# Kernel tuning notes

Hardware: AMD Instinct MI355X
Metric: run time of the kernel (lower is better)

The kernel has to match this reference:

```python
import jax, jax.numpy as jnp
import numpy as np

B, L, C, D = 8, 8192, 256, 256


def setup_inputs() -> dict:
    key = jax.random.key(0)
    ks = jax.random.split(key, 13)
    bound = 1.0 / np.sqrt(C)

    def W(k):
        return jax.random.uniform(k, (C, D), jnp.float32, -bound, bound)

    def b(k):
        return jax.random.uniform(k, (D,), jnp.float32, -bound, bound)

    return {
        "xs": jax.random.normal(ks[0], (B, L, C), jnp.float32),
        # forward-direction params
        "Wh1": W(ks[1]), "bh1": b(ks[2]),
        "Wz1": W(ks[3]), "bz1": b(ks[4]),
        "Ws1": W(ks[5]), "bs1": b(ks[6]),
        "h01": jnp.zeros((1, 1, D), jnp.float32),
        # backward-direction params
        "Wh_1": W(ks[7]), "bh_1": b(ks[8]),
        "Wz_1": W(ks[9]), "bz_1": b(ks[10]),
        "Ws_1": W(ks[11]), "bs_1": b(ks[12]),
        "h0_1": jnp.zeros((1, 1, D), jnp.float32),
    }


def _gru_scan(z, h_tilde, h0):
    """h[t] = z[t]*h_tilde[t] + (1-z[t])*h[t-1], h[-1]=h0. Parallel over time
    via associative scan on the affine maps h -> a*h + b."""
    a = 1.0 - z            # [B, L, D]
    b = z * h_tilde        # [B, L, D]

    def combine(c1, c2):
        a1, b1 = c1
        a2, b2 = c2
        return a1 * a2, a2 * b1 + b2

    A, Bc = jax.lax.associative_scan(combine, (a, b), axis=1)
    return Bc + A * h0     # broadcast h0 [1,1,D]


def reference(xs, Wh1, bh1, Wz1, bz1, Ws1, bs1, h01,
              Wh_1, bh_1, Wz_1, bz_1, Ws_1, bs_1, h0_1):
    sig = jax.nn.sigmoid
    # forward direction
    hf = _gru_scan(sig(xs @ Wz1 + bz1), xs @ Wh1 + bh1, h01) * sig(xs @ Ws1 + bs1)
    # backward direction: reverse time, scan, reverse back
    zr = sig(xs @ Wz_1 + bz_1)
    hr = xs @ Wh_1 + bh_1
    hb = _gru_scan(zr[:, ::-1], hr[:, ::-1], h0_1)[:, ::-1] * sig(xs @ Ws_1 + bs_1)
    return hf + hb
```

## Files before the change

### kernel.cpp

```cpp
#include <hip/hip_runtime.h>
#include <hip/hip_bf16.h>

typedef unsigned short u16;

#define BDIM 8
#define LDIM 8192
#define KDIM 256
#define DDIM 256
#define MTOT 65536
#define NDIM 1536
#define TCH  32
#define NCH  256


typedef float floatx4 __attribute__((ext_vector_type(4)));
typedef short bf16x8 __attribute__((ext_vector_type(8)));

__device__ __forceinline__ u16 f2bf(float f) {
  union { __hip_bfloat16 h; u16 u; } c;
  c.h = __float2bfloat16(f);
  return c.u;
}
__device__ __forceinline__ float bf2f(u16 u) {
  union { unsigned int i; float f; } c;
  c.i = ((unsigned int)u) << 16;
  return c.f;
}
__device__ __forceinline__ float sigmoidf_fast(float x) {
  return __builtin_amdgcn_rcpf(1.0f + __expf(-x));
}
__device__ __forceinline__ void gll16(const u16* g, u16* l) {
  __builtin_amdgcn_global_load_lds((const __attribute__((address_space(1))) void*)g,
                                   (__attribute__((address_space(3))) void*)l, 16, 0, 0);
}

__global__ void prep_weights(const float* __restrict__ Wh1, const float* __restrict__ Wz1,
                             const float* __restrict__ Ws1, const float* __restrict__ Wh_1,
                             const float* __restrict__ Wz_1, const float* __restrict__ Ws_1,
                             const float* __restrict__ bh1, const float* __restrict__ bz1,
                             const float* __restrict__ bs1, const float* __restrict__ bh_1,
                             const float* __restrict__ bz_1, const float* __restrict__ bs_1,
                             u16* __restrict__ WcatT, float* __restrict__ bcat) {
  const int n = blockIdx.x;
  const int k = threadIdx.x;
  const int dir = n / 768, r = n % 768;
  int d; const float* W; const float* bb;
  if (r < 512) {
    d = r >> 1;
    if (r & 1) { W = dir ? Wz_1 : Wz1; bb = dir ? bz_1 : bz1; }
    else       { W = dir ? Wh_1 : Wh1; bb = dir ? bh_1 : bh1; }
  } else {
    d = r - 512;
    W = dir ? Ws_1 : Ws1; bb = dir ? bs_1 : bs1;
  }
  WcatT[(size_t)n * KDIM + k] = f2bf(W[k * DDIM + d]);
  if (k == 0) bcat[n] = bb[d];
}

__global__ void convert_xs(const float* __restrict__ xs, u16* __restrict__ Abf) {
  size_t i = ((size_t)blockIdx.x * 256 + threadIdx.x) * 8;
  const float4* s = (const float4*)(xs + i);
  float4 f0 = s[0], f1 = s[1];
  union { u16 u[8]; uint4 v; } t;
  t.u[0] = f2bf(f0.x); t.u[1] = f2bf(f0.y); t.u[2] = f2bf(f0.z); t.u[3] = f2bf(f0.w);
  t.u[4] = f2bf(f1.x); t.u[5] = f2bf(f1.y); t.u[6] = f2bf(f1.z); t.u[7] = f2bf(f1.w);
  *(uint4*)(Abf + i) = t.v;
}

__global__ __launch_bounds__(256) void gemm_kernel(const u16* __restrict__ Abf,
                                                   const u16* __restrict__ WcatT,
                                                   const float* __restrict__ bcat,
                                                   u16* __restrict__ G) {
  __shared__ __align__(16) u16 As[8192];
  __shared__ __align__(16) u16 Bs[8192];
  const int tid = threadIdx.x;
  const int lane = tid & 63, wave = tid >> 6;
  const int wm = wave >> 1, wn = wave & 1;
  const int q = lane >> 4, r = lane & 15;

  const int xcd = blockIdx.x & 7;
  const int li  = blockIdx.x >> 3;
  const int mt  = xcd * 64 + li / 12;
  const int nt  = li % 12;
  const int m0 = mt * 128, n0 = nt * 128;

  const u16* gA[4]; const u16* gB[4]; u16* lA[4]; u16* lB[4];
#pragma unroll
  for (int j = 0; j < 4; j++) {
    const int bi = wave * 256 + j * 64 + lane;
    const int row = bi >> 3;
    const int kq = (bi & 7) ^ (row & 7);
    gA[j] = Abf   + (size_t)(m0 + row) * KDIM + kq * 8;
    gB[j] = WcatT + (size_t)(n0 + row) * KDIM + kq * 8;
    lA[j] = As + bi * 8;
    lB[j] = Bs + bi * 8;
  }

  floatx4 acc[4][4];
  floatx4 z4 = {0.f, 0.f, 0.f, 0.f};
#pragma unroll
  for (int i = 0; i < 4; i++)
#pragma unroll
    for (int j = 0; j < 4; j++) acc[i][j] = z4;

  for (int k0 = 0; k0 < KDIM; k0 += 64) {
#pragma unroll
    for (int j = 0; j < 4; j++) { gll16(gA[j] + k0, lA[j]); gll16(gB[j] + k0, lB[j]); }
    __syncthreads();
#pragma unroll
    for (int kk = 0; kk < 2; kk++) {
      bf16x8 af[4], bv[4];
#pragma unroll
      for (int i = 0; i < 4; i++) {
        const int row = wm * 64 + i * 16 + r;
        af[i] = *(const bf16x8*)(As + (row * 8 + ((kk * 4 + q) ^ (row & 7))) * 8);
      }
#pragma unroll
      for (int j = 0; j < 4; j++) {
        const int row = wn * 64 + j * 16 + r;
        bv[j] = *(const bf16x8*)(Bs + (row * 8 + ((kk * 4 + q) ^ (row & 7))) * 8);
      }
#pragma unroll
      for (int i = 0; i < 4; i++)
#pragma unroll
        for (int j = 0; j < 4; j++)
          acc[i][j] = __builtin_amdgcn_mfma_f32_16x16x32_bf16(af[i], bv[j], acc[i][j], 0, 0, 0);
    }
    __syncthreads();
  }

  float bvals[4];
#pragma unroll
  for (int j = 0; j < 4; j++) bvals[j] = bcat[n0 + wn * 64 + j * 16 + r];
#pragma unroll
  for (int i = 0; i < 4; i++) {
#pragma unroll
    for (int reg = 0; reg < 4; reg++) {
      size_t grow = (size_t)(m0 + wm * 64 + i * 16 + q * 4 + reg);
      u16* dst = G + grow * NDIM + n0 + wn * 64 + r;
#pragma unroll
      for (int j = 0; j < 4; j++)
        dst[j * 16] = f2bf(acc[i][j][reg] + bvals[j]);
    }
  }
}

__global__ __launch_bounds__(256) void scan_phaseA(const u16* __restrict__ G,
                                                   float* __restrict__ Acc,
                                                   float* __restrict__ Bcc) {
  const int slot = threadIdx.x >> 6, lane = threadIdx.x & 63;
  const int w = blockIdx.x * 4 + slot;
  const int u = w >> 1, half = w & 1;
  const int c = u & 255, b = (u >> 8) & 7, dir = u >> 11;
  const int d0 = half * 128 + lane * 2;
  const u16* p0 = G + (size_t)b * LDIM * NDIM + dir * 768 + d0 * 2;
  float h0 = 0.f, h1 = 0.f, P0 = 1.f, P1 = 1.f;
#pragma unroll 4
  for (int i = 0; i < TCH; ++i) {
    const int t = dir ? (c * TCH + (TCH - 1 - i)) : (c * TCH + i);
    uint2 hz = *(const uint2*)(p0 + (size_t)t * NDIM);
    const u16* q = (const u16*)&hz;
    float z0 = sigmoidf_fast(bf2f(q[1]));
    float z1 = sigmoidf_fast(bf2f(q[3]));
    float a0 = 1.f - z0, a1 = 1.f - z1;
    h0 = fmaf(a0, h0, z0 * bf2f(q[0]));
    h1 = fmaf(a1, h1, z1 * bf2f(q[2]));
    P0 *= a0; P1 *= a1;
  }
  float2 v;
  v.x = P0; v.y = P1;
  *(float2*)(Acc + (size_t)u * 256 + d0) = v;
  v.x = h0; v.y = h1;
  *(float2*)(Bcc + (size_t)u * 256 + d0) = v;
}

__global__ void scan_phaseB(const float* __restrict__ Acc, const float* __restrict__ Bcc,
                            const float* __restrict__ h01, const float* __restrict__ h0_1,
                            float* __restrict__ Pref) {
  const int d = threadIdx.x, b = blockIdx.x, dir = blockIdx.y;
  float h = dir ? h0_1[d] : h01[d];
  const size_t ubase = ((size_t)dir * BDIM + b) * NCH;
  if (dir == 0) {
    for (int c0 = 0; c0 < NCH; c0 += 8) {
      float a[8], bb[8];
#pragma unroll
      for (int j = 0; j < 8; ++j) {
        size_t idx = (ubase + c0 + j) * DDIM + d;
        a[j] = Acc[idx]; bb[j] = Bcc[idx];
      }
#pragma unroll
      for (int j = 0; j < 8; ++j) {
        Pref[(ubase + c0 + j) * DDIM + d] = h;
        h = fmaf(a[j], h, bb[j]);
      }
    }
  } else {
    for (int c0 = NCH - 1; c0 >= 0; c0 -= 8) {
      float a[8], bb[8];
#pragma unroll
      for (int j = 0; j < 8; ++j) {
        size_t idx = (ubase + c0 - j) * DDIM + d;
        a[j] = Acc[idx]; bb[j] = Bcc[idx];
      }
#pragma unroll
      for (int j = 0; j < 8; ++j) {
        Pref[(ubase + c0 - j) * DDIM + d] = h;
        h = fmaf(a[j], h, bb[j]);
      }
    }
  }
}

__global__ __launch_bounds__(512) void scan_phaseC(const u16* __restrict__ G,
                                                   const float* __restrict__ Pref,
                                                   float* __restrict__ out) {
  __shared__ float obuf[TCH * 256];
  const int c = blockIdx.x & 255, b = blockIdx.x >> 8;
  const int wave = threadIdx.x >> 6, lane = threadIdx.x & 63;
  const int dir = wave >> 2;
  const int d0 = (wave & 3) * 64 + lane;
  const int u = dir * 2048 + b * 256 + c;
  float h = Pref[(size_t)u * 256 + d0];
  const u16* ghz = G + (size_t)b * LDIM * NDIM + dir * 768 + d0 * 2;
  const u16* gs  = G + (size_t)b * LDIM * NDIM + dir * 768 + 512 + d0;

  if (dir == 1) {
#pragma unroll
    for (int i = 0; i < TCH; ++i) {
      const int tl = TCH - 1 - i;
      const int t = c * TCH + tl;
      unsigned int hz = *(const unsigned int*)(ghz + (size_t)t * NDIM);
      u16 sv = gs[(size_t)t * NDIM];
      float z = sigmoidf_fast(bf2f((u16)(hz >> 16)));
      h = fmaf(1.f - z, h, z * bf2f((u16)(hz & 0xffff)));
      obuf[tl * 256 + d0] = h * sigmoidf_fast(bf2f(sv));
    }
    __syncthreads();
  } else {
    float ov[TCH];
#pragma unroll
    for (int i = 0; i < TCH; ++i) {
      const int t = c * TCH + i;
      unsigned int hz = *(const unsigned int*)(ghz + (size_t)t * NDIM);
      u16 sv = gs[(size_t)t * NDIM];
      float z = sigmoidf_fast(bf2f((u16)(hz >> 16)));
      h = fmaf(1.f - z, h, z * bf2f((u16)(hz & 0xffff)));
      ov[i] = h * sigmoidf_fast(bf2f(sv));
    }
    __syncthreads();
#pragma unroll
    for (int i = 0; i < TCH; ++i) {
      const int t = c * TCH + i;
      out[((size_t)b * LDIM + t) * DDIM + d0] = ov[i] + obuf[i * 256 + d0];
    }
  }
}

extern "C" void kernel_launch(void* const* d_in, const int* in_sizes, int n_in,
                              void* d_out, int out_size, void* d_ws, size_t ws_size,
                              hipStream_t stream) {
  const float* xs   = (const float*)d_in[0];
  const float* Wh1  = (const float*)d_in[1];
  const float* bh1  = (const float*)d_in[2];
  const float* Wz1  = (const float*)d_in[3];
  const float* bz1  = (const float*)d_in[4];
  const float* Ws1  = (const float*)d_in[5];
  const float* bs1  = (const float*)d_in[6];
  const float* h01  = (const float*)d_in[7];
  const float* Wh_1 = (const float*)d_in[8];
  const float* bh_1 = (const float*)d_in[9];
  const float* Wz_1 = (const float*)d_in[10];
  const float* bz_1 = (const float*)d_in[11];
  const float* Ws_1 = (const float*)d_in[12];
  const float* bs_1 = (const float*)d_in[13];
  const float* h0_1 = (const float*)d_in[14];
  float* out = (float*)d_out;

  char* ws = (char*)d_ws;
  u16* WcatT = (u16*)ws;   ws += (size_t)NDIM * KDIM * 2;
  float* bcat = (float*)ws; ws += (size_t)NDIM * 4;
  u16* Abf = (u16*)ws;     ws += (size_t)MTOT * KDIM * 2;
  u16* G = (u16*)ws;       ws += (size_t)MTOT * NDIM * 2;
  float* Acc  = (float*)Abf;
  float* Bcc  = Acc + (size_t)2 * BDIM * NCH * DDIM;
  float* Pref = Bcc + (size_t)2 * BDIM * NCH * DDIM;
  if ((size_t)(ws - (char*)d_ws) > ws_size) return;

  prep_weights<<<dim3(NDIM), dim3(KDIM), 0, stream>>>(
      Wh1, Wz1, Ws1, Wh_1, Wz_1, Ws_1, bh1, bz1, bs1, bh_1, bz_1, bs_1, WcatT, bcat);
  convert_xs<<<dim3(MTOT * KDIM / (256 * 8)), dim3(256), 0, stream>>>(xs, Abf);
  gemm_kernel<<<dim3(6144), dim3(256), 0, stream>>>(Abf, WcatT, bcat, G);
  scan_phaseA<<<dim3(2048), dim3(256), 0, stream>>>(G, Acc, Bcc);
  scan_phaseB<<<dim3(BDIM, 2), dim3(DDIM), 0, stream>>>(Acc, Bcc, h01, h0_1, Pref);
  scan_phaseC<<<dim3(2048), dim3(512), 0, stream>>>(G, Pref, out);
}
```

Baseline: 298.8 us.

## Fuse chunk-local scan phase A into GEMM epilogue with permuted weight columns

Permutes the concatenated weight columns so each lane's four MFMA outputs are contiguous, which allows vectorized uint2 stores of G and a float4 bias load. For h/z column tiles, the GEMM epilogue also stages the bf16 tile in shared memory and computes the per-chunk scan products and offsets directly. This removes the separate scan_phaseA launch and its re-read of G. In exchange it adds a shared-memory pass and a serial 32-step loop to the epilogue of those tiles. It only runs when the workspace has room for separate Acc/Bcc buffers.

After: 284.2 us. 1.05x faster.

```diff
diff --git a/kernel.cpp b/kernel.cpp
--- a/kernel.cpp
+++ b/kernel.cpp
@@ -43,7 +43,9 @@
                              u16* __restrict__ WcatT, float* __restrict__ bcat) {
   const int n = blockIdx.x;
   const int k = threadIdx.x;
-  const int dir = n / 768, r = n % 768;
+  const int nn = n & 63;
+  const int p = (n & ~63) | ((nn & 15) << 2) | (nn >> 4);
+  const int dir = p / 768, r = p % 768;
   int d; const float* W; const float* bb;
   if (r < 512) {
     d = r >> 1;
@@ -54,7 +56,7 @@
     W = dir ? Ws_1 : Ws1; bb = dir ? bs_1 : bs1;
   }
   WcatT[(size_t)n * KDIM + k] = f2bf(W[k * DDIM + d]);
-  if (k == 0) bcat[n] = bb[d];
+  if (k == 0) bcat[p] = bb[d];
 }
 
 __global__ void convert_xs(const float* __restrict__ xs, u16* __restrict__ Abf) {
@@ -70,9 +72,13 @@
 __global__ __launch_bounds__(256) void gemm_kernel(const u16* __restrict__ Abf,
                                                    const u16* __restrict__ WcatT,
                                                    const float* __restrict__ bcat,
-                                                   u16* __restrict__ G) {
-  __shared__ __align__(16) u16 As[8192];
-  __shared__ __align__(16) u16 Bs[8192];
+                                                   u16* __restrict__ G,
+                                                   float* __restrict__ Acc,
+                                                   float* __restrict__ Bcc,
+                                                   int fuse) {
+  __shared__ __align__(16) u16 sm[16384];
+  u16* As = sm;
+  u16* Bs = sm + 8192;
   const int tid = threadIdx.x;
   const int lane = tid & 63, wave = tid >> 6;
   const int wm = wave >> 1, wn = wave & 1;
@@ -129,19 +135,45 @@
     __syncthreads();
   }
 
-  float bvals[4];
-#pragma unroll
-  for (int j = 0; j < 4; j++) bvals[j] = bcat[n0 + wn * 64 + j * 16 + r];
+  const int pcol = wn * 64 + (r << 2);
+  const float4 bv4 = *(const float4*)(bcat + n0 + pcol);
+  const int hz = fuse && ((n0 % 768) < 512);
 #pragma unroll
   for (int i = 0; i < 4; i++) {
 #pragma unroll
     for (int reg = 0; reg < 4; reg++) {
-      size_t grow = (size_t)(m0 + wm * 64 + i * 16 + q * 4 + reg);
-      u16* dst = G + grow * NDIM + n0 + wn * 64 + r;
-#pragma unroll
-      for (int j = 0; j < 4; j++)
-        dst[j * 16] = f2bf(acc[i][j][reg] + bvals[j]);
-    }
+      const int lrow = wm * 64 + i * 16 + q * 4 + reg;
+      union { u16 u[4]; uint2 v; } t;
+      t.u[0] = f2bf(acc[i][0][reg] + bv4.x);
+      t.u[1] = f2bf(acc[i][1][reg] + bv4.y);
+      t.u[2] = f2bf(acc[i][2][reg] + bv4.z);
+      t.u[3] = f2bf(acc[i][3][reg] + bv4.w);
+      *(uint2*)(G + (size_t)(m0 + lrow) * NDIM + n0 + pcol) = t.v;
+      if (hz) *(uint2*)(sm + lrow * 128 + pcol) = t.v;
+    }
+  }
+
+  if (hz) {
+    __syncthreads();
+    const int cc = wave;
+    const int dd = lane;
+    const int dirn = n0 / 768;
+    const int dbase = (n0 % 768) >> 1;
+    const int bb = m0 >> 13;
+    const int c0 = (m0 & 8191) >> 5;
+    float h = 0.f, P = 1.f;
+#pragma unroll 8
+    for (int i = 0; i < TCH; ++i) {
+      const int tl = dirn ? (TCH - 1 - i) : i;
+      const unsigned int hzv = *(const unsigned int*)(sm + (cc * 32 + tl) * 128 + dd * 2);
+      const float z = sigmoidf_fast(bf2f((u16)(hzv >> 16)));
+      const float a = 1.f - z;
+      h = fmaf(a, h, z * bf2f((u16)(hzv & 0xffffu)));
+      P *= a;
+    }
+    const size_t u = (size_t)dirn * 2048 + (size_t)bb * 256 + (size_t)(c0 + cc);
+    Acc[u * 256 + dbase + dd] = P;
+    Bcc[u * 256 + dbase + dd] = h;
   }
 }
 
@@ -281,16 +313,29 @@
   float* bcat = (float*)ws; ws += (size_t)NDIM * 4;
   u16* Abf = (u16*)ws;     ws += (size_t)MTOT * KDIM * 2;
   u16* G = (u16*)ws;       ws += (size_t)MTOT * NDIM * 2;
-  float* Acc  = (float*)Abf;
-  float* Bcc  = Acc + (size_t)2 * BDIM * NCH * DDIM;
-  float* Pref = Bcc + (size_t)2 * BDIM * NCH * DDIM;
-  if ((size_t)(ws - (char*)d_ws) > ws_size) return;
+
+  const size_t sumElems = (size_t)2 * BDIM * NCH * DDIM;
+  float* Acc; float* Bcc; float* Pref;
+  int fuse;
+  if ((size_t)(ws - (char*)d_ws) + 3 * sumElems * 4 <= ws_size) {
+    Acc  = (float*)ws;
+    Bcc  = Acc + sumElems;
+    Pref = Bcc + sumElems;
+    fuse = 1;
+  } else {
+    if ((size_t)(ws - (char*)d_ws) > ws_size) return;
+    Acc  = (float*)Abf;
+    Bcc  = Acc + sumElems;
+    Pref = Bcc + sumElems;
+    fuse = 0;
+  }
 
   prep_weights<<<dim3(NDIM), dim3(KDIM), 0, stream>>>(
       Wh1, Wz1, Ws1, Wh_1, Wz_1, Ws_1, bh1, bz1, bs1, bh_1, bz_1, bs_1, WcatT, bcat);
   convert_xs<<<dim3(MTOT * KDIM / (256 * 8)), dim3(256), 0, stream>>>(xs, Abf);
-  gemm_kernel<<<dim3(6144), dim3(256), 0, stream>>>(Abf, WcatT, bcat, G);
-  scan_phaseA<<<dim3(2048), dim3(256), 0, stream>>>(G, Acc, Bcc);
+  gemm_kernel<<<dim3(6144), dim3(256), 0, stream>>>(Abf, WcatT, bcat, G, Acc, Bcc, fuse);
+  if (!fuse)
+    scan_phaseA<<<dim3(2048), dim3(256), 0, stream>>>(G, Acc, Bcc);
   scan_phaseB<<<dim3(BDIM, 2), dim3(DDIM), 0, stream>>>(Acc, Bcc, h01, h0_1, Pref);
   scan_phaseC<<<dim3(2048), dim3(512), 0, stream>>>(G, Pref, out);
 }
```
